# Kernel optimization log

Measured on AMD Instinct MI355X. Metric: run time of the kernel, lower is better.

## Reference

```python
import jax, jax.numpy as jnp
import numpy as np

HIDDEN = 512
EXP = 2048  # hidden * expansion_factor(4)

def _glorot(key, shape):
    fan_in = shape[0]
    return jax.random.normal(key, shape, dtype=jnp.float32) / np.sqrt(fan_in)

def setup_inputs() -> dict:
    key = jax.random.key(0)
    ks = jax.random.split(key, 6)
    B, S = 4, 4096
    return {
        "x": jax.random.normal(ks[0], (B, S, HIDDEN), dtype=jnp.float32),
        "W_in1": _glorot(ks[1], (HIDDEN, EXP)),
        "b_in1": jnp.zeros((EXP,), jnp.float32),
        "W_in2": _glorot(ks[2], (HIDDEN, EXP)),
        "b_in2": jnp.zeros((EXP,), jnp.float32),
        "W_z": _glorot(ks[3], (EXP, EXP)),
        "b_z": jnp.zeros((EXP,), jnp.float32),
        "W_h": _glorot(ks[4], (EXP, EXP)),
        "b_h": jnp.zeros((EXP,), jnp.float32),
        "W_out": _glorot(ks[5], (EXP, HIDDEN)),
        "b_out": jnp.zeros((HIDDEN,), jnp.float32),
    }

def _min_gru(x_in, W_z, b_z, W_h, b_h):
    # minGRU: h_t = (1 - z_t) * h_{t-1} + z_t * h_tilde_t, h_0 = 0
    z = jax.nn.sigmoid(jnp.einsum("bse,ef->bsf", x_in, W_z) + b_z)
    h_tilde = jnp.einsum("bse,ef->bsf", x_in, W_h) + b_h
    a = 1.0 - z          # decay coeff
    b = z * h_tilde      # input term
    def combine(c1, c2):
        a1, b1 = c1
        a2, b2 = c2
        return (a1 * a2, b1 * a2 + b2)
    _, h = jax.lax.associative_scan(combine, (a, b), axis=1)
    return h

def reference(x, W_in1, b_in1, W_in2, b_in2, W_z, b_z, W_h, b_h, W_out, b_out):
    x_in = jax.nn.silu(jnp.einsum("bsd,de->bse", x, W_in1) + b_in1)
    x_skip = jax.nn.silu(jnp.einsum("bsd,de->bse", x, W_in2) + b_in2)
    h = _min_gru(x_in, W_z, b_z, W_h, b_h)
    return jnp.einsum("bse,ed->bsd", x_skip + h, W_out) + b_out
```

## Files before the change

kernel.cpp:

```cpp
#include <hip/hip_runtime.h>
#include <hip/hip_bf16.h>


typedef __bf16 bf16x8 __attribute__((ext_vector_type(8)));
typedef __bf16 bf16x4 __attribute__((ext_vector_type(4)));
typedef float  f32x4  __attribute__((ext_vector_type(4)));

#define DEVINL __device__ __forceinline__

DEVINL void async_ld16(const __bf16* g, __bf16* l) {
    __builtin_amdgcn_global_load_lds(
        (const __attribute__((address_space(1))) void*)g,
        (__attribute__((address_space(3))) void*)l, 16, 0, 0);
}

DEVINL float fsigmoid(float v) { return 1.0f / (1.0f + __expf(-v)); }

template <int MODE>
__global__ __launch_bounds__(512, 4)
void gemm4(const __bf16* __restrict__ A, const __bf16* __restrict__ Bt,
           const float* __restrict__ bias, const float* __restrict__ bias2,
           void* __restrict__ out, void* __restrict__ out2, int N, int K,
           int bps, int seg_stride, int row_off)
{
    struct KL { __bf16 A[128 * 32]; __bf16 B[256 * 32]; };
    __shared__ union SM4 {
        KL kl[2];
        __bf16 ct[64 * 264];
    } sm;
    const int tid = threadIdx.x;
    const int bx = blockIdx.x;
    const int seg = bx / bps;
    const int within = bx - seg * bps;
    const int gm0 = row_off + seg * seg_stride + within * 128;
    const int om0 = bx * 128;
    const int n0 = blockIdx.y * 256;

    const int rA = tid >> 2,         kA = (tid & 3) ^ ((tid >> 3) & 3);
    const int c0 = tid, c1 = tid + 512;
    const int rB0 = c0 >> 2,         kB0 = (c0 & 3) ^ ((c0 >> 3) & 3);
    const int rB1 = c1 >> 2,         kB1 = (c1 & 3) ^ ((c1 >> 3) & 3);
    const __bf16* Ag  = A  + (size_t)(gm0 + rA)  * K + kA  * 8;
    const __bf16* Bg0 = Bt + (size_t)(n0 + rB0) * K + kB0 * 8;
    const __bf16* Bg1 = Bt + (size_t)(n0 + rB1) * K + kB1 * 8;

    const int lane = tid & 63;
    const int wave = tid >> 6;
    const int wm = wave >> 2;
    const int wn = wave & 3;
    const int quad = lane >> 4;
    const int r = lane & 15;
    const int swz = (quad ^ ((r >> 1) & 3)) * 8;

    f32x4 acc[4][4] = {};

    const int T = K >> 5;

    auto stage = [&](int t, int b) {
        const int kt = t << 5;
        async_ld16(Ag  + kt, sm.kl[b].A + tid * 8);
        async_ld16(Bg0 + kt, sm.kl[b].B + c0 * 8);
        async_ld16(Bg1 + kt, sm.kl[b].B + c1 * 8);
    };

    stage(0, 0);

    for (int t = 0; t < T; ++t) {
        const int cur = t & 1;
        if (t + 1 < T) {
            stage(t + 1, cur ^ 1);
            asm volatile("s_waitcnt vmcnt(3)\n\ts_barrier" ::: "memory");
        } else {
            asm volatile("s_waitcnt vmcnt(0)\n\ts_barrier" ::: "memory");
        }

        const __bf16* ap = sm.kl[cur].A + (wm * 64 + r) * 32 + swz;
        const __bf16* bp = sm.kl[cur].B + (wn * 64 + r) * 32 + swz;
        bf16x8 af[4], bf_[4];
#pragma unroll
        for (int m = 0; m < 4; ++m) af[m] = *(const bf16x8*)(ap + m * 512);
#pragma unroll
        for (int n = 0; n < 4; ++n) bf_[n] = *(const bf16x8*)(bp + n * 512);

        __builtin_amdgcn_s_setprio(1);
#pragma unroll
        for (int m = 0; m < 4; ++m)
#pragma unroll
            for (int n = 0; n < 4; ++n)
                acc[m][n] = __builtin_amdgcn_mfma_f32_16x16x32_bf16(
                    af[m], bf_[n], acc[m][n], 0, 0, 0);
        __builtin_amdgcn_s_setprio(0);

        asm volatile("s_waitcnt lgkmcnt(0)\n\ts_barrier" ::: "memory");
    }

    const bool lo = n0 < 2048;
    __bf16* dst;
    int cb;
    size_t stride;
    if (MODE == 0) {
        dst = lo ? (__bf16*)out : (__bf16*)out2;
        cb = lo ? n0 : n0 - 2048;
        stride = 2048;
    } else {
        dst = (__bf16*)out;
        cb = n0;
        stride = (size_t)N;
    }
    float bvj[4];
#pragma unroll
    for (int nf = 0; nf < 4; ++nf) {
        const int gc = n0 + wn * 64 + nf * 16 + r;
        bvj[nf] = lo ? bias[gc] : bias2[gc - 2048];
    }

#pragma unroll
    for (int p = 0; p < 2; ++p) {
        if (wm == p) {
#pragma unroll
            for (int mm = 0; mm < 4; ++mm)
#pragma unroll
                for (int nf = 0; nf < 4; ++nf)
#pragma unroll
                    for (int k = 0; k < 4; ++k) {
                        const float v = acc[mm][nf][k] + bvj[nf];
                        const __bf16 o = (MODE == 0) ? (__bf16)(v * fsigmoid(v))
                                                     : (__bf16)v;
                        sm.ct[(mm * 16 + quad * 4 + k) * 264 +
                              (wn * 64 + nf * 16 + r)] = o;
                    }
        }
        __syncthreads();
#pragma unroll
        for (int q = 0; q < 4; ++q) {
            const int chunk = q * 512 + tid;
            const int trow = chunk >> 5;
            const int tc = (chunk & 31) * 8;
            const bf16x8 vv = *(const bf16x8*)(sm.ct + trow * 264 + tc);
            *(bf16x8*)(dst + (size_t)(om0 + p * 64 + trow) * stride + cb + tc) = vv;
        }
        __syncthreads();
    }
}

template <int MODE>
__global__ __launch_bounds__(512, 2)
void gemm3k(const __bf16* __restrict__ A, const __bf16* __restrict__ Bt,
            const float* __restrict__ bias, const float* __restrict__ bias2,
            void* __restrict__ out, void* __restrict__ out2, int N, int K,
            int bps, int seg_stride, int row_off)
{
    struct KL { __bf16 A[256 * 64]; __bf16 B[256 * 64]; };
    __shared__ union SM3K {
        KL kl[2];
        __bf16 ct[64 * 264];
    } sm;
    const int tid = threadIdx.x;
    const int bx = blockIdx.x;
    const int seg = bx / bps;
    const int within = bx - seg * bps;
    const int gm0 = row_off + seg * seg_stride + within * 256;
    const int om0 = bx * 256;
    const int n0 = blockIdx.y * 256;

    int rA[4], kA[4];
#pragma unroll
    for (int j = 0; j < 4; ++j) {
        const int s = tid + 512 * j;
        rA[j] = s >> 3;
        kA[j] = (s & 7) ^ (rA[j] & 7);
    }
    const __bf16* Agp[4];
    const __bf16* Bgp[4];
#pragma unroll
    for (int j = 0; j < 4; ++j) {
        Agp[j] = A  + (size_t)(gm0 + rA[j]) * K + kA[j] * 8;
        Bgp[j] = Bt + (size_t)(n0 + rA[j]) * K + kA[j] * 8;
    }

    const int lane = tid & 63;
    const int wave = tid >> 6;
    const int wm = wave >> 2;
    const int wn = wave & 3;
    const int quad = lane >> 4;
    const int r = lane & 15;

    f32x4 acc[8][4] = {};

    const int T = K >> 6;

    auto stage = [&](int t, int b) {
        const int kt = t << 6;
#pragma unroll
        for (int j = 0; j < 4; ++j)
            async_ld16(Agp[j] + kt, sm.kl[b].A + (tid + 512 * j) * 8);
#pragma unroll
        for (int j = 0; j < 4; ++j)
            async_ld16(Bgp[j] + kt, sm.kl[b].B + (tid + 512 * j) * 8);
    };

    stage(0, 0);

    const int swz0 = ((0 * 4 + quad) ^ (r & 7)) * 8;
    const int swz1 = ((1 * 4 + quad) ^ (r & 7)) * 8;

    for (int t = 0; t < T; ++t) {
        const int cur = t & 1;
        const bool pre = (t + 1) < T;
        const __bf16* apb = sm.kl[cur].A + (wm * 128 + r) * 64;
        const __bf16* bpb = sm.kl[cur].B + (wn * 64 + r) * 64;

        bf16x8 bfr[2][4];

        if (pre) {
            stage(t + 1, cur ^ 1);
            asm volatile("s_waitcnt vmcnt(8)" ::: "memory");
        } else {
            asm volatile("s_waitcnt vmcnt(0)" ::: "memory");
        }
        __builtin_amdgcn_s_barrier();
        {
            bf16x8 a00 = *(const bf16x8*)(apb + 0 * 1024 + swz0);
            bf16x8 a01 = *(const bf16x8*)(apb + 0 * 1024 + swz1);
            bf16x8 a10 = *(const bf16x8*)(apb + 1 * 1024 + swz0);
            bf16x8 a11 = *(const bf16x8*)(apb + 1 * 1024 + swz1);
#pragma unroll
            for (int n = 0; n < 4; ++n) {
                bfr[0][n] = *(const bf16x8*)(bpb + n * 1024 + swz0);
                bfr[1][n] = *(const bf16x8*)(bpb + n * 1024 + swz1);
            }
            asm volatile("s_waitcnt lgkmcnt(0)" ::: "memory");
            __builtin_amdgcn_s_setprio(1);
#pragma unroll
            for (int n = 0; n < 4; ++n) {
                acc[0][n] = __builtin_amdgcn_mfma_f32_16x16x32_bf16(a00, bfr[0][n], acc[0][n], 0, 0, 0);
                acc[0][n] = __builtin_amdgcn_mfma_f32_16x16x32_bf16(a01, bfr[1][n], acc[0][n], 0, 0, 0);
                acc[1][n] = __builtin_amdgcn_mfma_f32_16x16x32_bf16(a10, bfr[0][n], acc[1][n], 0, 0, 0);
                acc[1][n] = __builtin_amdgcn_mfma_f32_16x16x32_bf16(a11, bfr[1][n], acc[1][n], 0, 0, 0);
            }
            __builtin_amdgcn_s_setprio(0);
        }
        __builtin_amdgcn_s_barrier();

#pragma unroll
        for (int p = 1; p < 4; ++p) {
            bf16x8 a00 = *(const bf16x8*)(apb + (2 * p    ) * 1024 + swz0);
            bf16x8 a01 = *(const bf16x8*)(apb + (2 * p    ) * 1024 + swz1);
            bf16x8 a10 = *(const bf16x8*)(apb + (2 * p + 1) * 1024 + swz0);
            bf16x8 a11 = *(const bf16x8*)(apb + (2 * p + 1) * 1024 + swz1);
            __builtin_amdgcn_s_barrier();
            asm volatile("s_waitcnt lgkmcnt(0)" ::: "memory");
            __builtin_amdgcn_s_setprio(1);
#pragma unroll
            for (int n = 0; n < 4; ++n) {
                acc[2 * p][n]     = __builtin_amdgcn_mfma_f32_16x16x32_bf16(a00, bfr[0][n], acc[2 * p][n], 0, 0, 0);
                acc[2 * p][n]     = __builtin_amdgcn_mfma_f32_16x16x32_bf16(a01, bfr[1][n], acc[2 * p][n], 0, 0, 0);
                acc[2 * p + 1][n] = __builtin_amdgcn_mfma_f32_16x16x32_bf16(a10, bfr[0][n], acc[2 * p + 1][n], 0, 0, 0);
                acc[2 * p + 1][n] = __builtin_amdgcn_mfma_f32_16x16x32_bf16(a11, bfr[1][n], acc[2 * p + 1][n], 0, 0, 0);
            }
            __builtin_amdgcn_s_setprio(0);
            __builtin_amdgcn_s_barrier();
        }
    }

    __syncthreads();

    const bool lo = n0 < 2048;
    __bf16* dst = (__bf16*)out;
    const int cb = n0;
    const size_t stride = (size_t)N;
    float bvj[4];
#pragma unroll
    for (int nf = 0; nf < 4; ++nf) {
        const int gc = n0 + wn * 64 + nf * 16 + r;
        bvj[nf] = lo ? bias[gc] : bias2[gc - 2048];
    }

#pragma unroll
    for (int p = 0; p < 4; ++p) {
        if (wm == (p >> 1)) {
            const int mb = (p & 1) * 4;
#pragma unroll
            for (int mm = 0; mm < 4; ++mm)
#pragma unroll
                for (int nf = 0; nf < 4; ++nf)
#pragma unroll
                    for (int k = 0; k < 4; ++k) {
                        const float v = acc[mb + mm][nf][k] + bvj[nf];
                        sm.ct[(mm * 16 + quad * 4 + k) * 264 +
                              (wn * 64 + nf * 16 + r)] = (__bf16)v;
                    }
        }
        __syncthreads();
#pragma unroll
        for (int q = 0; q < 4; ++q) {
            const int chunk = q * 512 + tid;
            const int trow = chunk >> 5;
            const int tc = (chunk & 31) * 8;
            const bf16x8 vv = *(const bf16x8*)(sm.ct + trow * 264 + tc);
            *(bf16x8*)(dst + (size_t)(om0 + p * 64 + trow) * stride + cb + tc) = vv;
        }
        __syncthreads();
    }
}

template <int MODE>
__global__ __launch_bounds__(256)
void gemm_bt64(const __bf16* __restrict__ A, const __bf16* __restrict__ Bt,
               const float* __restrict__ bias, const float* __restrict__ bias2,
               void* __restrict__ out, void* __restrict__ out2, int N, int K,
               int bps, int seg_stride, int row_off)
{
    struct KL64 { __bf16 A[128 * 64]; __bf16 B[128 * 64]; };
    __shared__ union SMB64 {
        KL64 kl[2];
        float  ctf[32 * 132];
    } sm;
    const int tid = threadIdx.x;
    const int bx = blockIdx.x;
    const int seg = bx / bps;
    const int within = bx - seg * bps;
    const int gm0 = row_off + seg * seg_stride + within * 128;
    const int om0 = bx * 128;
    const int n0 = blockIdx.y * 128;

    int rS[4], kS[4];
#pragma unroll
    for (int j = 0; j < 4; ++j) {
        const int s = tid + 256 * j;
        rS[j] = s >> 3;
        kS[j] = (s & 7) ^ (rS[j] & 7);
    }
    const __bf16* Agp[4];
    const __bf16* Bgp[4];
#pragma unroll
    for (int j = 0; j < 4; ++j) {
        Agp[j] = A  + (size_t)(gm0 + rS[j]) * K + kS[j] * 8;
        Bgp[j] = Bt + (size_t)(n0 + rS[j]) * K + kS[j] * 8;
    }

    const int lane = tid & 63;
    const int wave = tid >> 6;
    const int wrow = (wave >> 1) * 64;
    const int wcol = (wave & 1) * 64;
    const int quad = lane >> 4;
    const int r = lane & 15;

    f32x4 acc[4][4] = {};

    const int T = K >> 6;

    auto stage = [&](int t, int b) {
        const int kt = t << 6;
#pragma unroll
        for (int j = 0; j < 4; ++j)
            async_ld16(Agp[j] + kt, sm.kl[b].A + (tid + 256 * j) * 8);
#pragma unroll
        for (int j = 0; j < 4; ++j)
            async_ld16(Bgp[j] + kt, sm.kl[b].B + (tid + 256 * j) * 8);
    };

    stage(0, 0);

    const int swz0 = ((0 * 4 + quad) ^ (r & 7)) * 8;
    const int swz1 = ((1 * 4 + quad) ^ (r & 7)) * 8;

    for (int t = 0; t < T; ++t) {
        const int cur = t & 1;
        if (t + 1 < T) {
            stage(t + 1, cur ^ 1);
            asm volatile("s_waitcnt vmcnt(8)\n\ts_barrier" ::: "memory");
        } else {
            asm volatile("s_waitcnt vmcnt(0)\n\ts_barrier" ::: "memory");
        }

        const __bf16* apb = sm.kl[cur].A + (wrow + r) * 64;
        const __bf16* bpb = sm.kl[cur].B + (wcol + r) * 64;

#pragma unroll
        for (int ks = 0; ks < 2; ++ks) {
            const int swz = ks ? swz1 : swz0;
            bf16x8 af[4], bf_[4];
#pragma unroll
            for (int m = 0; m < 4; ++m)
                af[m] = *(const bf16x8*)(apb + m * 1024 + swz);
#pragma unroll
            for (int n = 0; n < 4; ++n)
                bf_[n] = *(const bf16x8*)(bpb + n * 1024 + swz);

            __builtin_amdgcn_s_setprio(1);
#pragma unroll
            for (int m = 0; m < 4; ++m)
#pragma unroll
                for (int n = 0; n < 4; ++n)
                    acc[m][n] = __builtin_amdgcn_mfma_f32_16x16x32_bf16(
                        af[m], bf_[n], acc[m][n], 0, 0, 0);
            __builtin_amdgcn_s_setprio(0);
        }

        asm volatile("s_waitcnt lgkmcnt(0)\n\ts_barrier" ::: "memory");
    }

    {
        float bvj[4];
#pragma unroll
        for (int j = 0; j < 4; ++j)
            bvj[j] = bias[n0 + wcol + j * 16 + r];
#pragma unroll
        for (int p = 0; p < 4; ++p) {
#pragma unroll
            for (int j = 0; j < 4; ++j)
#pragma unroll
                for (int k = 0; k < 4; ++k)
                    sm.ctf[((wave >> 1) * 16 + quad * 4 + k) * 132 +
                           (wcol + j * 16 + r)] = acc[p][j][k] + bvj[j];
            __syncthreads();
#pragma unroll
            for (int q = 0; q < 4; ++q) {
                const int chunk = q * 256 + tid;
                const int trow = chunk >> 5;
                const int tc4 = (chunk & 31) * 4;
                const f32x4 vv = *(const f32x4*)(sm.ctf + trow * 132 + tc4);
                const int grow = om0 + (trow >> 4) * 64 + p * 16 + (trow & 15);
                *(f32x4*)((float*)out + (size_t)grow * N + n0 + tc4) = vv;
            }
            __syncthreads();
        }
    }
}

#define SSEG 32
#define SCOLS 32
__global__ __launch_bounds__(1024)
void scan_kernel(const __bf16* __restrict__ raw, __bf16* __restrict__ xskip,
                 float* __restrict__ carry, int CS, int S, int t0, int first)
{
    __shared__ float Als[SSEG][SCOLS];
    __shared__ float Bls[SSEG][SCOLS];
    const int lane = threadIdx.x & (SCOLS - 1);
    const int w = threadIdx.x >> 5;
    const int nb8 = gridDim.x >> 3;
    const int lin = (blockIdx.x & 7) * nb8 + (blockIdx.x >> 3);
    const int gpb = 2048 / SCOLS;
    const int batch = lin / gpb;
    const int col = (lin - batch * gpb) * SCOLS + lane;
    const int L = CS / SSEG;
    const int tbeg = w * L;

    const size_t rbase = ((size_t)batch * CS + tbeg) * 4096 + col;

    float av[32], bv[32];
    float A = 1.0f, Bv = 0.0f;
    {
        size_t idx = rbase;
#pragma unroll
        for (int t = 0; t < 32; ++t, idx += 4096) {
            const float z = fsigmoid((float)raw[idx]);
            const float b = z * (float)raw[idx + 2048];
            const float a = 1.0f - z;
            av[t] = a;
            bv[t] = b;
            Bv = a * Bv + b;
            A *= a;
        }
    }
    Als[w][lane] = A;
    Bls[w][lane] = Bv;
    __syncthreads();

    const int ch = batch * 2048 + col;
    float h = first ? 0.0f : carry[ch];
    for (int s = 0; s < w; ++s)
        h = Als[s][lane] * h + Bls[s][lane];
    if (w == SSEG - 1)
        carry[ch] = A * h + Bv;

    {
        size_t gidx = ((size_t)batch * S + t0 + tbeg) * 2048 + col;
#pragma unroll
        for (int t = 0; t < 32; ++t, gidx += 2048) {
            h = av[t] * h + bv[t];
            xskip[gidx] = (__bf16)((float)xskip[gidx] + h);
        }
    }
}

__global__ __launch_bounds__(256)
void prep_kernel(const float* __restrict__ x, __bf16* __restrict__ xb,
                 const float* __restrict__ W_in1, const float* __restrict__ W_in2,
                 __bf16* __restrict__ Wt12,
                 const float* __restrict__ W_z, const float* __restrict__ W_h,
                 __bf16* __restrict__ Wtzh,
                 const float* __restrict__ W_out, __bf16* __restrict__ Wto)
{
    __shared__ float tile[32][33];
    int bid = blockIdx.x;
    if (bid < 8192) {
        const int i = bid * 256 + threadIdx.x;
        const float4 v = ((const float4*)x)[i];
        bf16x4 o;
        o[0] = (__bf16)v.x; o[1] = (__bf16)v.y;
        o[2] = (__bf16)v.z; o[3] = (__bf16)v.w;
        ((bf16x4*)xb)[i] = o;
        return;
    }
    bid -= 8192;
    const float* W;
    __bf16* dst;
    int K, N, nb, kb;
    if (bid < 2048) {
        const int z = bid >> 10, rem = bid & 1023;
        W = z ? W_in2 : W_in1;
        dst = Wt12 + (size_t)z * 512 * 2048;
        K = 512; N = 2048;
        nb = (rem & 63) * 32; kb = (rem >> 6) * 32;
    } else if (bid < 2048 + 8192) {
        const int b2 = bid - 2048;
        const int z = b2 >> 12, rem = b2 & 4095;
        W = z ? W_h : W_z;
        dst = Wtzh + (size_t)z * 2048 * 2048;
        K = 2048; N = 2048;
        nb = (rem & 63) * 32; kb = (rem >> 6) * 32;
    } else {
        const int b3 = bid - (2048 + 8192);
        W = W_out; dst = Wto;
        K = 2048; N = 512;
        nb = (b3 & 15) * 32; kb = (b3 >> 4) * 32;
    }
    const int tx = threadIdx.x & 31;
    const int ty = threadIdx.x >> 5;
#pragma unroll
    for (int i = 0; i < 32; i += 8)
        tile[ty + i][tx] = W[(size_t)(kb + ty + i) * N + nb + tx];
    __syncthreads();
#pragma unroll
    for (int i = 0; i < 32; i += 8)
        dst[(size_t)(nb + ty + i) * K + kb + tx] = (__bf16)tile[tx][ty + i];
}

extern "C" void kernel_launch(void* const* d_in, const int* in_sizes, int n_in,
                              void* d_out, int out_size, void* d_ws, size_t ws_size,
                              hipStream_t stream)
{
    const float* x     = (const float*)d_in[0];
    const float* W_in1 = (const float*)d_in[1];
    const float* b_in1 = (const float*)d_in[2];
    const float* W_in2 = (const float*)d_in[3];
    const float* b_in2 = (const float*)d_in[4];
    const float* W_z   = (const float*)d_in[5];
    const float* b_z   = (const float*)d_in[6];
    const float* W_h   = (const float*)d_in[7];
    const float* b_h   = (const float*)d_in[8];
    const float* W_out = (const float*)d_in[9];
    const float* b_out = (const float*)d_in[10];

    const int B = 4, S = 4096, H = 512, E = 2048;
    const int M = B * S;
    const int CS = 1024;
    const int NC = S / CS;
    const int MC = B * CS;

    const size_t MiB = 1024 * 1024;
    const size_t NEEDED = 183 * MiB;
    if (ws_size < NEEDED) return;

    char* ws = (char*)d_ws;
    __bf16* xb    = (__bf16*)(ws + 0);
    __bf16* rawzh = (__bf16*)(ws + 0);
    float*  carry = (float*) (ws + 32 * MiB);
    __bf16* xin   = (__bf16*)(ws + 33 * MiB);
    __bf16* xskip = (__bf16*)(ws + 97 * MiB);
    __bf16* Wt12  = (__bf16*)(ws + 161 * MiB);
    __bf16* Wtzh  = (__bf16*)(ws + 165 * MiB);
    __bf16* Wto   = (__bf16*)(ws + 181 * MiB);

    prep_kernel<<<8192 + 2048 + 8192 + 1024, 256, 0, stream>>>(
        x, xb, W_in1, W_in2, Wt12, W_z, W_h, Wtzh, W_out, Wto);

    gemm4<0><<<dim3(M / 128, 2 * E / 256), 512, 0, stream>>>(
        xb, Wt12, b_in1, b_in2, xin, xskip, 2 * E, H, M / 128, 0, 0);

    for (int c = 0; c < NC; ++c) {
        const int row_off = c * CS;
        gemm3k<4><<<dim3(MC / 256, 2 * E / 256), 512, 0, stream>>>(
            xin, Wtzh, b_z, b_h, rawzh, nullptr, 2 * E, E, CS / 256, S, row_off);
        scan_kernel<<<(B * E) / SCOLS, 1024, 0, stream>>>(
            rawzh, xskip, carry, CS, S, row_off, c == 0);
    }

    gemm_bt64<3><<<dim3(M / 128, H / 128), 256, 0, stream>>>(
        xskip, Wto, b_out, nullptr, (float*)d_out, nullptr, H, E, M / 128, 0, 0);
}
```

Measured before the change: 599.6 us.

## Split A-tile prefetch into per-phase chunks interleaved with MFMA phases

The A-tile global-to-LDS loads are split into four 32-row chunks, each matching the rows a compute phase reads. The next tile's chunks are issued inside the phase loop and fine-grained vmcnt waits are added, so each phase waits only for its own rows instead of the whole tile. This spreads memory issue across the compute phases and lets MFMA start before the full A tile lands. It adds fragile vmcnt bookkeeping that must match exact issue counts.

```diff
diff --git a/kernel.cpp b/kernel.cpp
--- a/kernel.cpp
+++ b/kernel.cpp
@@ -163,20 +163,23 @@
     const int om0 = bx * 256;
     const int n0 = blockIdx.y * 256;
 
-    int rA[4], kA[4];
+    int rB[4], kB[4];
 #pragma unroll
     for (int j = 0; j < 4; ++j) {
         const int s = tid + 512 * j;
-        rA[j] = s >> 3;
-        kA[j] = (s & 7) ^ (rA[j] & 7);
-    }
-    const __bf16* Agp[4];
+        rB[j] = s >> 3;
+        kB[j] = (s & 7) ^ (rB[j] & 7);
+    }
     const __bf16* Bgp[4];
 #pragma unroll
-    for (int j = 0; j < 4; ++j) {
-        Agp[j] = A  + (size_t)(gm0 + rA[j]) * K + kA[j] * 8;
-        Bgp[j] = Bt + (size_t)(n0 + rA[j]) * K + kA[j] * 8;
-    }
+    for (int j = 0; j < 4; ++j)
+        Bgp[j] = Bt + (size_t)(n0 + rB[j]) * K + kB[j] * 8;
+
+    const int lr = tid >> 3;
+    const int rowOff = (lr < 32) ? lr : (96 + lr);
+    const int posA = tid & 7;
+    const int kcA = posA ^ (rowOff & 7);
+    const __bf16* AgS = A + (size_t)(gm0 + rowOff) * K + kcA * 8;
 
     const int lane = tid & 63;
     const int wave = tid >> 6;
@@ -189,17 +192,21 @@
 
     const int T = K >> 6;
 
-    auto stage = [&](int t, int b) {
+    auto issueB = [&](int t, int b) {
         const int kt = t << 6;
-#pragma unroll
-        for (int j = 0; j < 4; ++j)
-            async_ld16(Agp[j] + kt, sm.kl[b].A + (tid + 512 * j) * 8);
 #pragma unroll
         for (int j = 0; j < 4; ++j)
             async_ld16(Bgp[j] + kt, sm.kl[b].B + (tid + 512 * j) * 8);
     };
-
-    stage(0, 0);
+    auto issueA = [&](int t, int b, int p) {
+        const int kt = t << 6;
+        async_ld16(AgS + (size_t)(32 * p) * K + kt,
+                   sm.kl[b].A + ((rowOff + 32 * p) * 8 + posA) * 8);
+    };
+
+    issueB(0, 0);
+#pragma unroll
+    for (int p = 0; p < 4; ++p) issueA(0, 0, p);
 
     const int swz0 = ((0 * 4 + quad) ^ (r & 7)) * 8;
     const int swz1 = ((1 * 4 + quad) ^ (r & 7)) * 8;
@@ -213,10 +220,10 @@
         bf16x8 bfr[2][4];
 
         if (pre) {
-            stage(t + 1, cur ^ 1);
-            asm volatile("s_waitcnt vmcnt(8)" ::: "memory");
+            issueB(t + 1, cur ^ 1);
+            asm volatile("s_waitcnt vmcnt(7)" ::: "memory");
         } else {
-            asm volatile("s_waitcnt vmcnt(0)" ::: "memory");
+            asm volatile("s_waitcnt vmcnt(3)" ::: "memory");
         }
         __builtin_amdgcn_s_barrier();
         {
@@ -240,6 +247,8 @@
             }
             __builtin_amdgcn_s_setprio(0);
         }
+        if (pre) asm volatile("s_waitcnt vmcnt(6)" ::: "memory");
+        else     asm volatile("s_waitcnt vmcnt(2)" ::: "memory");
         __builtin_amdgcn_s_barrier();
 
 #pragma unroll
@@ -248,6 +257,11 @@
             bf16x8 a01 = *(const bf16x8*)(apb + (2 * p    ) * 1024 + swz1);
             bf16x8 a10 = *(const bf16x8*)(apb + (2 * p + 1) * 1024 + swz0);
             bf16x8 a11 = *(const bf16x8*)(apb + (2 * p + 1) * 1024 + swz1);
+            if (pre) {
+                if (p == 1) { issueA(t + 1, cur ^ 1, 0); issueA(t + 1, cur ^ 1, 1); }
+                else if (p == 2) issueA(t + 1, cur ^ 1, 2);
+                else issueA(t + 1, cur ^ 1, 3);
+            }
             __builtin_amdgcn_s_barrier();
             asm volatile("s_waitcnt lgkmcnt(0)" ::: "memory");
             __builtin_amdgcn_s_setprio(1);
@@ -259,6 +273,13 @@
                 acc[2 * p + 1][n] = __builtin_amdgcn_mfma_f32_16x16x32_bf16(a11, bfr[1][n], acc[2 * p + 1][n], 0, 0, 0);
             }
             __builtin_amdgcn_s_setprio(0);
+            if (p == 1) {
+                if (pre) asm volatile("s_waitcnt vmcnt(7)" ::: "memory");
+                else     asm volatile("s_waitcnt vmcnt(1)" ::: "memory");
+            } else if (p == 2) {
+                if (pre) asm volatile("s_waitcnt vmcnt(7)" ::: "memory");
+                else     asm volatile("s_waitcnt vmcnt(0)" ::: "memory");
+            }
             __builtin_amdgcn_s_barrier();
         }
     }
```

Measured after the change: 590.9 us. No clear change (-1.4%).
